# Optimization experiments

Measured on AMD Instinct MI355X. Metric: run time of the kernel, lower is better.

Reference implementation:

```python
import jax, jax.numpy as jnp
import numpy as np

B, S, K = 128, 196, 512   # batch, encoder seq, keys_hidden_size
T_CAP = 16                # caption length (out_seq_len = 15)
V, E, H = 32000, 512, 512 # vocab, embedding, hidden


def setup_inputs() -> dict:
    key = jax.random.key(0)
    ks = jax.random.split(key, 16)
    sc = lambda fan_in: 1.0 / np.sqrt(fan_in)
    return {
        "features": jax.random.normal(ks[0], (B, S, K), jnp.float32),
        "captions": jax.random.randint(ks[1], (B, T_CAP), 0, V),
        "emb": jax.random.normal(ks[2], (V, E), jnp.float32) * 0.02,
        "fc1_w": jax.random.normal(ks[3], (H, E), jnp.float32) * sc(E),
        "fc1_b": jnp.zeros((H,), jnp.float32),
        "att_wq": jax.random.normal(ks[4], (H, H), jnp.float32) * sc(H),
        "att_wk": jax.random.normal(ks[5], (H, K), jnp.float32) * sc(K),
        "att_v": jax.random.normal(ks[6], (H,), jnp.float32) * sc(H),
        "fc0_w": jax.random.normal(ks[7], (H, K), jnp.float32) * sc(K),
        "fc0_b": jnp.zeros((H,), jnp.float32),
        "gru_wih": jax.random.normal(ks[8], (3 * H, 2 * H), jnp.float32) * sc(2 * H),
        "gru_whh": jax.random.normal(ks[9], (3 * H, H), jnp.float32) * sc(H),
        "gru_bih": jnp.zeros((3 * H,), jnp.float32),
        "gru_bhh": jnp.zeros((3 * H,), jnp.float32),
        "fc2_w": jax.random.normal(ks[10], (V, H), jnp.float32) * sc(H),
        "fc2_b": jnp.zeros((V,), jnp.float32),
    }


def reference(features, captions, emb, fc1_w, fc1_b, att_wq, att_wk, att_v,
              fc0_w, fc0_b, gru_wih, gru_whh, gru_bih, gru_bhh, fc2_w, fc2_b):
    # embed captions and project: (B, T_CAP, H)
    x = emb[captions] @ fc1_w.T + fc1_b
    # precompute key projection for Bahdanau attention: (B, S, H)
    keys_proj = features @ att_wk.T

    def step(h, x_t):
        # Bahdanau additive attention
        q = h @ att_wq.T                                   # (B, H)
        scores = jnp.tanh(q[:, None, :] + keys_proj) @ att_v  # (B, S)
        w = jax.nn.softmax(scores, axis=1)
        context = jnp.einsum('bs,bsk->bk', w, features)    # (B, K)
        context = context @ fc0_w.T + fc0_b                # fc_0 -> (B, H)
        rnn_in = jnp.concatenate([x_t, context], axis=-1)  # (B, 2H)
        # GRU cell, torch gate order (r, z, n)
        gi = rnn_in @ gru_wih.T + gru_bih
        gh = h @ gru_whh.T + gru_bhh
        ir, iz, inn = jnp.split(gi, 3, axis=-1)
        hr, hz, hn = jnp.split(gh, 3, axis=-1)
        r = jax.nn.sigmoid(ir + hr)
        z = jax.nn.sigmoid(iz + hz)
        n = jnp.tanh(inn + r * hn)
        h_new = (1.0 - z) * n + z * h
        out = h_new @ fc2_w.T + fc2_b                      # fc_2 -> (B, V)
        return h_new, out

    out_seq_len = captions.shape[1] - 1
    xs = jnp.swapaxes(x[:, :out_seq_len], 0, 1)            # (T, B, H)
    h0 = jnp.zeros((features.shape[0], fc0_b.shape[0]), features.dtype)
    _, outs = jax.lax.scan(step, h0, xs)                   # (T, B, V)
    return jnp.swapaxes(outs, 0, 1)                        # (B, T, V)
```

## Files before the change

### kernel.cpp

```cpp
#include <hip/hip_runtime.h>

typedef _Float16 half_t;
typedef float    floatx4 __attribute__((ext_vector_type(4)));
typedef _Float16 halfx8  __attribute__((ext_vector_type(8)));
typedef _Float16 halfx2  __attribute__((ext_vector_type(2)));

__device__ __forceinline__ float tanh_f(float x) {
  float e = __expf(2.0f * x);
  return 1.0f - 2.0f / (e + 1.0f);
}
__device__ __forceinline__ float sigmoid_f(float x) {
  return 1.0f / (1.0f + __expf(-x));
}

__device__ __forceinline__ void gl16(const void* g, void* s) {
  __builtin_amdgcn_global_load_lds((__attribute__((address_space(1))) unsigned int*)g,
                                   (__attribute__((address_space(3))) unsigned int*)s,
                                   16, 0, 0);
}

__device__ __forceinline__ int xcd_swz(int bid, int nwg) {
  int q = nwg >> 3, r = nwg & 7, x = bid & 7, p = bid >> 3;
  return (x < r ? x * (q + 1) : r * (q + 1) + (x - r) * q) + p;
}

__global__ __launch_bounds__(256) void k_cvt_f16(const float* __restrict__ src,
                                                 half_t* __restrict__ dst, int n) {
  int i = (blockIdx.x * 256 + threadIdx.x) * 4;
  if (i < n) {
    float4 v = *(const float4*)(src + i);
    halfx2 a; a[0] = (half_t)v.x; a[1] = (half_t)v.y;
    halfx2 b; b[0] = (half_t)v.z; b[1] = (half_t)v.w;
    *(halfx2*)(dst + i) = a;
    *(halfx2*)(dst + i + 2) = b;
  }
}

__global__ __launch_bounds__(256) void k_wihsplit(const float* __restrict__ wih,
                                                  half_t* __restrict__ wx,
                                                  half_t* __restrict__ wc) {
  int row = blockIdx.x, j = threadIdx.x * 2;
  float2 a = *(const float2*)(wih + (size_t)row * 1024 + j);
  float2 b = *(const float2*)(wih + (size_t)row * 1024 + 512 + j);
  halfx2 ax; ax[0] = (half_t)a.x; ax[1] = (half_t)a.y;
  halfx2 bx; bx[0] = (half_t)b.x; bx[1] = (half_t)b.y;
  *(halfx2*)(wx + (size_t)row * 512 + j) = ax;
  *(halfx2*)(wc + (size_t)row * 512 + j) = bx;
}

__global__ __launch_bounds__(256) void k_gather(const float* __restrict__ emb,
                                                const int* __restrict__ cap,
                                                half_t* __restrict__ dst) {
  int row = blockIdx.x;
  int b = row / 15, t = row - b * 15;
  int c = cap[b * 16 + t];
  const float* s = emb + (size_t)c * 512;
  int e = threadIdx.x * 2;
  float2 v = *(const float2*)(s + e);
  halfx2 o; o[0] = (half_t)v.x; o[1] = (half_t)v.y;
  *(halfx2*)(dst + (size_t)row * 512 + e) = o;
}

__global__ __launch_bounds__(256) void k_biasc(const float* __restrict__ fc0b,
                                               float* __restrict__ biasc) {
  int i = blockIdx.x * 256 + threadIdx.x;
  biasc[i] = (i < 512) ? 0.f : fc0b[i - 512];
}

__global__ __launch_bounds__(256) void k_zero(float4* p) {
  p[blockIdx.x * 256 + threadIdx.x] = make_float4(0.f, 0.f, 0.f, 0.f);
}

template <bool OUT_F16>
__device__ __forceinline__ void gemm128_body(const half_t* __restrict__ Ap,
                                             const half_t* __restrict__ Bp,
                                             const float* __restrict__ bias,
                                             void* __restrict__ Cp,
                                             const int Kd, const int ldc,
                                             const int m0, const int n0) {
  constexpr int ABYTES = 128 * 32 * 2;
  constexpr int BBYTES = 128 * 32 * 2;
  __shared__ __align__(16) char smem[2 * ABYTES + 2 * BBYTES];

  const int l = threadIdx.x & 63;
  const int w = threadIdx.x >> 6;

  const half_t* gA = Ap + (size_t)(m0 + w * 32 + (l >> 2)) * Kd + (l & 3) * 8;
  const half_t* gB = Bp + (size_t)(n0 + w * 32 + (l >> 2)) * Kd + (l & 3) * 8;

  const int fr = l & 15;
  const int kq = (l >> 4) * 8;
  const int mh = (w & 1) * 64;
  const int nh = (w >> 1) * 64;

  floatx4 acc[4][4];
#pragma unroll
  for (int i = 0; i < 4; ++i)
#pragma unroll
    for (int j = 0; j < 4; ++j) { floatx4 z = {0.f, 0.f, 0.f, 0.f}; acc[i][j] = z; }

  const int NT = Kd >> 5;

  auto stage = [&](int tt) {
    const int k0 = tt * 32;
    char* aD = smem + (tt & 1) * ABYTES;
    char* bD = smem + 2 * ABYTES + (tt & 1) * BBYTES;
    const half_t* g = gA + k0;
    gl16(g, aD + (w * 32) * 64);
    gl16(g + (size_t)16 * Kd, aD + (w * 32 + 16) * 64);
    const half_t* g2 = gB + k0;
    gl16(g2, bD + (w * 32) * 64);
    gl16(g2 + (size_t)16 * Kd, bD + (w * 32 + 16) * 64);
  };

  stage(0);

  for (int t = 0; t < NT; ++t) {
    __syncthreads();
    if (t + 1 < NT) stage(t + 1);
    const char* aB = smem + (t & 1) * ABYTES;
    const char* bB = smem + 2 * ABYTES + (t & 1) * BBYTES;
    halfx8 af[4], bf[4];
#pragma unroll
    for (int i = 0; i < 4; ++i) {
      af[i] = *(const halfx8*)((const half_t*)aB + (size_t)(mh + i * 16 + fr) * 32 + kq);
      bf[i] = *(const halfx8*)((const half_t*)bB + (size_t)(nh + i * 16 + fr) * 32 + kq);
    }
#pragma unroll
    for (int i = 0; i < 4; ++i)
#pragma unroll
      for (int j = 0; j < 4; ++j)
        acc[i][j] = __builtin_amdgcn_mfma_f32_16x16x32_f16(af[i], bf[j], acc[i][j], 0, 0, 0);
  }

#pragma unroll
  for (int j = 0; j < 4; ++j) {
    const int n = n0 + nh + j * 16 + fr;
    const float bv = bias ? bias[n] : 0.0f;
#pragma unroll
    for (int i = 0; i < 4; ++i) {
      const int mb = m0 + mh + i * 16 + (l >> 4) * 4;
#pragma unroll
      for (int r = 0; r < 4; ++r) {
        const float v = acc[i][j][r] + bv;
        const size_t ci = (size_t)(mb + r) * ldc + n;
        if constexpr (OUT_F16) ((half_t*)Cp)[ci] = (half_t)v;
        else                   ((float*)Cp)[ci] = v;
      }
    }
  }
}

template <bool OUT_F16>
__global__ __launch_bounds__(256) void k_gemm_lds(const half_t* __restrict__ Ap,
                                                  const half_t* __restrict__ Bp,
                                                  const float* __restrict__ bias,
                                                  void* __restrict__ Cp,
                                                  int Kd, int ldc) {
  gemm128_body<OUT_F16>(Ap, Bp, bias, Cp, Kd, ldc,
                        blockIdx.y * 128, blockIdx.x * 128);
}

__global__ __launch_bounds__(256) void k_kpfp(const half_t* __restrict__ featf,
                                              const half_t* __restrict__ wkfc0,
                                              const float* __restrict__ biasc,
                                              half_t* __restrict__ kpfp) {
  const int w = (blockIdx.x & 7) * 196 + (blockIdx.x >> 3);
  const int n0 = (w & 7) * 128;
  const int m0 = (w >> 3) * 128;
  gemm128_body<true>(featf, wkfc0, biasc, kpfp, 512, 1024, m0, n0);
}

__global__ __launch_bounds__(256) void k_fc2_final(const half_t* __restrict__ hall,
                                                   const half_t* __restrict__ fc2w,
                                                   const float* __restrict__ fc2b,
                                                   float* __restrict__ outp) {
  const int w = xcd_swz(blockIdx.x, 3750);
  const int m0 = (w % 15) * 128;
  const int n0 = (w / 15) * 128;
  gemm128_body<false>(hall, fc2w, fc2b, outp, 512, 32000, m0, n0);
}

__global__ __launch_bounds__(256) void k_scores(const half_t* __restrict__ kpfp,
                                                const float* __restrict__ ghq,
                                                const float* __restrict__ attv,
                                                float* __restrict__ scores) {
  int w = blockIdx.x * 4 + (threadIdx.x >> 6);
  int l = threadIdx.x & 63;
  int b = w / 196;
  halfx8 kv = *(const halfx8*)(kpfp + (size_t)w * 1024 + l * 8);
  const float* qr = ghq + (size_t)b * 2048 + 1536 + l * 8;
  float4 q0 = *(const float4*)qr;
  float4 q1 = *(const float4*)(qr + 4);
  float4 a0 = *(const float4*)(attv + l * 8);
  float4 a1 = *(const float4*)(attv + l * 8 + 4);
  float acc = a0.x * tanh_f(q0.x + (float)kv[0]);
  acc += a0.y * tanh_f(q0.y + (float)kv[1]);
  acc += a0.z * tanh_f(q0.z + (float)kv[2]);
  acc += a0.w * tanh_f(q0.w + (float)kv[3]);
  acc += a1.x * tanh_f(q1.x + (float)kv[4]);
  acc += a1.y * tanh_f(q1.y + (float)kv[5]);
  acc += a1.z * tanh_f(q1.z + (float)kv[6]);
  acc += a1.w * tanh_f(q1.w + (float)kv[7]);
#pragma unroll
  for (int off = 32; off > 0; off >>= 1) acc += __shfl_xor(acc, off, 64);
  if (l == 0) scores[w] = acc;
}

__global__ __launch_bounds__(256) void k_ctx(const float* __restrict__ scores,
                                             const half_t* __restrict__ kpfp,
                                             half_t* __restrict__ ctxo) {
  const int b = blockIdx.x, kt = blockIdx.y * 128, t = threadIdx.x;
  __shared__ float sw[196], red[256];
  float sc = (t < 196) ? scores[b * 196 + t] : -1e30f;
  red[t] = sc; __syncthreads();
  for (int o = 128; o > 0; o >>= 1) { if (t < o) red[t] = fmaxf(red[t], red[t + o]); __syncthreads(); }
  float mx = red[0]; __syncthreads();
  float e = (t < 196) ? __expf(sc - mx) : 0.f;
  red[t] = e; __syncthreads();
  for (int o = 128; o > 0; o >>= 1) { if (t < o) red[t] += red[t + o]; __syncthreads(); }
  float inv = 1.0f / red[0];
  if (t < 196) sw[t] = e * inv;
  __syncthreads();
  const int kk = t & 127, half = t >> 7, s0 = half * 98;
  const half_t* fp = kpfp + (size_t)(b * 196 + s0) * 1024 + 512 + kt + kk;
  float acc = 0.f;
#pragma unroll 7
  for (int i = 0; i < 98; ++i) acc += sw[s0 + i] * (float)fp[(size_t)i * 1024];
  red[t] = acc; __syncthreads();
  if (t < 128) ctxo[(size_t)b * 512 + kt + t] = (half_t)(red[t] + red[t + 128]);
}

__global__ __launch_bounds__(256) void k_gates(const float* __restrict__ gix,
                                               const float* __restrict__ gic,
                                               const float* __restrict__ ghq,
                                               const float* __restrict__ bih,
                                               const float* __restrict__ bhh,
                                               float* __restrict__ hbuf,
                                               half_t* __restrict__ hh,
                                               half_t* __restrict__ hall, int step) {
  int idx = blockIdx.x * 256 + threadIdx.x;
  int b = idx >> 9, n = idx & 511;
  const float* gx = gix + (size_t)(b * 15 + step) * 1536;
  const float* gc = gic + (size_t)b * 1536;
  const float* gh = ghq + (size_t)b * 2048;
  float ir  = gx[n]        + gc[n]        + bih[n];
  float iz  = gx[n + 512]  + gc[n + 512]  + bih[n + 512];
  float in_ = gx[n + 1024] + gc[n + 1024] + bih[n + 1024];
  float hr  = gh[n]        + bhh[n];
  float hz  = gh[n + 512]  + bhh[n + 512];
  float hn  = gh[n + 1024] + bhh[n + 1024];
  float r = sigmoid_f(ir + hr);
  float z = sigmoid_f(iz + hz);
  float nn = tanh_f(in_ + r * hn);
  float hv = (1.0f - z) * nn + z * hbuf[idx];
  hbuf[idx] = hv;
  half_t h16 = (half_t)hv;
  hh[idx] = h16;
  hall[(size_t)(b * 15 + step) * 512 + n] = h16;
}

extern "C" void kernel_launch(void* const* d_in, const int* in_sizes, int n_in,
                              void* d_out, int out_size, void* d_ws, size_t ws_size,
                              hipStream_t stream) {
  (void)in_sizes; (void)n_in; (void)out_size; (void)ws_size;
  const float* features = (const float*)d_in[0];
  const int*   captions = (const int*)d_in[1];
  const float* emb      = (const float*)d_in[2];
  const float* fc1_w    = (const float*)d_in[3];
  const float* fc1_b    = (const float*)d_in[4];
  const float* att_wq   = (const float*)d_in[5];
  const float* att_wk   = (const float*)d_in[6];
  const float* att_v    = (const float*)d_in[7];
  const float* fc0_w    = (const float*)d_in[8];
  const float* fc0_b    = (const float*)d_in[9];
  const float* gru_wih  = (const float*)d_in[10];
  const float* gru_whh  = (const float*)d_in[11];
  const float* gru_bih  = (const float*)d_in[12];
  const float* gru_bhh  = (const float*)d_in[13];
  const float* fc2_w    = (const float*)d_in[14];
  const float* fc2_b    = (const float*)d_in[15];
  float* out = (float*)d_out;

  char* p = (char*)d_ws;
  half_t* kpfp   = (half_t*)p; p += (size_t)25088 * 1024 * 2;
  half_t* fc2w_h = (half_t*)p; p += (size_t)32000 * 512 * 2;
  float*  gix    = (float*)p;  p += (size_t)1920 * 1536 * 4;
  half_t* wihx_h = (half_t*)p; p += (size_t)1536 * 512 * 2;
  half_t* wihc_h = (half_t*)p; p += (size_t)1536 * 512 * 2;
  half_t* bcat2  = (half_t*)p; p += (size_t)2048 * 512 * 2;
  half_t* wkfc0  = (half_t*)p; p += (size_t)1024 * 512 * 2;
  half_t* fc1w_h = (half_t*)p; p += (size_t)512 * 512 * 2;
  half_t* embg_h = (half_t*)p; p += (size_t)1920 * 512 * 2;
  half_t* xproj_h= (half_t*)p; p += (size_t)1920 * 512 * 2;
  float*  biasc  = (float*)p;  p += (size_t)1024 * 4;
  float*  ghq    = (float*)p;  p += (size_t)128 * 2048 * 4;
  float*  hbuf   = (float*)p;  p += (size_t)128 * 512 * 4;
  float*  scores = (float*)p;  p += (size_t)128 * 196 * 4;
  float*  gic    = (float*)p;  p += (size_t)128 * 1536 * 4;
  half_t* ctxo   = (half_t*)p; p += (size_t)128 * 512 * 2;
  half_t* h_h    = (half_t*)p; p += (size_t)128 * 512 * 2;
  half_t* featf  = (half_t*)p; p += (size_t)25088 * 512 * 2;
  half_t* hall   = (half_t*)p; p += (size_t)1920 * 512 * 2;

  k_cvt_f16<<<dim3(16000), 256, 0, stream>>>(fc2_w, fc2w_h, 32000 * 512);
  k_cvt_f16<<<dim3(12544), 256, 0, stream>>>(features, featf, 25088 * 512);
  k_cvt_f16<<<dim3(256),   256, 0, stream>>>(fc1_w, fc1w_h, 512 * 512);
  k_cvt_f16<<<dim3(256),   256, 0, stream>>>(att_wk, wkfc0, 512 * 512);
  k_cvt_f16<<<dim3(256),   256, 0, stream>>>(fc0_w, wkfc0 + (size_t)512 * 512, 512 * 512);
  k_cvt_f16<<<dim3(768),   256, 0, stream>>>(gru_whh, bcat2, 1536 * 512);
  k_cvt_f16<<<dim3(256),   256, 0, stream>>>(att_wq, bcat2 + (size_t)1536 * 512, 512 * 512);
  k_wihsplit<<<dim3(1536), 256, 0, stream>>>(gru_wih, wihx_h, wihc_h);
  k_gather<<<dim3(1920), 256, 0, stream>>>(emb, captions, embg_h);
  k_biasc<<<dim3(4), 256, 0, stream>>>(fc0_b, biasc);
  k_zero<<<dim3(320), 256, 0, stream>>>((float4*)ghq);
  k_gemm_lds<true><<<dim3(4, 15), 256, 0, stream>>>(embg_h, fc1w_h, fc1_b, xproj_h, 512, 512);
  k_kpfp<<<dim3(1568), 256, 0, stream>>>(featf, wkfc0, biasc, kpfp);
  k_gemm_lds<false><<<dim3(12, 15), 256, 0, stream>>>(xproj_h, wihx_h, nullptr, gix, 512, 1536);

  for (int t = 0; t < 15; ++t) {
    k_scores<<<dim3(6272), 256, 0, stream>>>(kpfp, ghq, att_v, scores);
    k_ctx<<<dim3(128, 4), 256, 0, stream>>>(scores, kpfp, ctxo);
    k_gemm_lds<false><<<dim3(12, 1), 256, 0, stream>>>(ctxo, wihc_h, nullptr, gic, 512, 1536);
    k_gates<<<dim3(256), 256, 0, stream>>>(gix, gic, ghq, gru_bih, gru_bhh, hbuf, h_h, hall, t);
    k_gemm_lds<false><<<dim3(16, 1), 256, 0, stream>>>(h_h, bcat2, nullptr, ghq, 512, 2048);
  }
  k_fc2_final<<<dim3(3750), 256, 0, stream>>>(hall, fc2w_h, fc2_b, out);
}
```

Baseline: 1.206 ms.

## Fuse recurrent decode loop into one persistent kernel with grid barriers

Replaces the 75 per-step launches (scores, context, two small GEMMs, gates) with a single persistent kernel of 128 blocks, one per batch row. The blocks synchronise through an atomic grid barrier placed in the workspace and zeroed by the existing zero kernel. Attention scores, softmax and context for a batch row are now computed inside one block, and the GEMM body takes shared memory as a parameter so it can be reused. This removes launch gaps and intermediate round trips. In exchange the attention phase runs on only 128 CUs, the barriers spin, and correctness relies on all blocks being co-resident.

```diff
diff --git a/kernel.cpp b/kernel.cpp
--- a/kernel.cpp
+++ b/kernel.cpp
@@ -22,6 +22,22 @@
 __device__ __forceinline__ int xcd_swz(int bid, int nwg) {
   int q = nwg >> 3, r = nwg & 7, x = bid & 7, p = bid >> 3;
   return (x < r ? x * (q + 1) : r * (q + 1) + (x - r) * q) + p;
+}
+
+__device__ __forceinline__ void gbar(int* cnt, int* gen, int nb) {
+  __syncthreads();
+  if (threadIdx.x == 0) {
+    int g = __hip_atomic_load(gen, __ATOMIC_RELAXED, __HIP_MEMORY_SCOPE_AGENT);
+    if (__hip_atomic_fetch_add(cnt, 1, __ATOMIC_ACQ_REL, __HIP_MEMORY_SCOPE_AGENT) == nb - 1) {
+      __hip_atomic_store(cnt, 0, __ATOMIC_RELAXED, __HIP_MEMORY_SCOPE_AGENT);
+      __hip_atomic_store(gen, g + 1, __ATOMIC_RELEASE, __HIP_MEMORY_SCOPE_AGENT);
+    } else {
+      while (__hip_atomic_load(gen, __ATOMIC_ACQUIRE, __HIP_MEMORY_SCOPE_AGENT) == g) {
+        __builtin_amdgcn_s_sleep(8);
+      }
+    }
+  }
+  __syncthreads();
 }
 
 __global__ __launch_bounds__(256) void k_cvt_f16(const float* __restrict__ src,
@@ -77,10 +93,10 @@
                                              const float* __restrict__ bias,
                                              void* __restrict__ Cp,
                                              const int Kd, const int ldc,
-                                             const int m0, const int n0) {
+                                             const int m0, const int n0,
+                                             char* smem) {
   constexpr int ABYTES = 128 * 32 * 2;
   constexpr int BBYTES = 128 * 32 * 2;
-  __shared__ __align__(16) char smem[2 * ABYTES + 2 * BBYTES];
 
   const int l = threadIdx.x & 63;
   const int w = threadIdx.x >> 6;
@@ -132,6 +148,7 @@
       for (int j = 0; j < 4; ++j)
         acc[i][j] = __builtin_amdgcn_mfma_f32_16x16x32_f16(af[i], bf[j], acc[i][j], 0, 0, 0);
   }
+  __syncthreads();
 
 #pragma unroll
   for (int j = 0; j < 4; ++j) {
@@ -157,107 +174,142 @@
                                                   const float* __restrict__ bias,
                                                   void* __restrict__ Cp,
                                                   int Kd, int ldc) {
+  __shared__ __align__(16) char smem[32768];
   gemm128_body<OUT_F16>(Ap, Bp, bias, Cp, Kd, ldc,
-                        blockIdx.y * 128, blockIdx.x * 128);
+                        blockIdx.y * 128, blockIdx.x * 128, smem);
 }
 
 __global__ __launch_bounds__(256) void k_kpfp(const half_t* __restrict__ featf,
                                               const half_t* __restrict__ wkfc0,
                                               const float* __restrict__ biasc,
                                               half_t* __restrict__ kpfp) {
+  __shared__ __align__(16) char smem[32768];
   const int w = (blockIdx.x & 7) * 196 + (blockIdx.x >> 3);
   const int n0 = (w & 7) * 128;
   const int m0 = (w >> 3) * 128;
-  gemm128_body<true>(featf, wkfc0, biasc, kpfp, 512, 1024, m0, n0);
+  gemm128_body<true>(featf, wkfc0, biasc, kpfp, 512, 1024, m0, n0, smem);
 }
 
 __global__ __launch_bounds__(256) void k_fc2_final(const half_t* __restrict__ hall,
                                                    const half_t* __restrict__ fc2w,
                                                    const float* __restrict__ fc2b,
                                                    float* __restrict__ outp) {
+  __shared__ __align__(16) char smem[32768];
   const int w = xcd_swz(blockIdx.x, 3750);
   const int m0 = (w % 15) * 128;
   const int n0 = (w / 15) * 128;
-  gemm128_body<false>(hall, fc2w, fc2b, outp, 512, 32000, m0, n0);
-}
-
-__global__ __launch_bounds__(256) void k_scores(const half_t* __restrict__ kpfp,
-                                                const float* __restrict__ ghq,
-                                                const float* __restrict__ attv,
-                                                float* __restrict__ scores) {
-  int w = blockIdx.x * 4 + (threadIdx.x >> 6);
-  int l = threadIdx.x & 63;
-  int b = w / 196;
-  halfx8 kv = *(const halfx8*)(kpfp + (size_t)w * 1024 + l * 8);
-  const float* qr = ghq + (size_t)b * 2048 + 1536 + l * 8;
-  float4 q0 = *(const float4*)qr;
-  float4 q1 = *(const float4*)(qr + 4);
-  float4 a0 = *(const float4*)(attv + l * 8);
-  float4 a1 = *(const float4*)(attv + l * 8 + 4);
-  float acc = a0.x * tanh_f(q0.x + (float)kv[0]);
-  acc += a0.y * tanh_f(q0.y + (float)kv[1]);
-  acc += a0.z * tanh_f(q0.z + (float)kv[2]);
-  acc += a0.w * tanh_f(q0.w + (float)kv[3]);
-  acc += a1.x * tanh_f(q1.x + (float)kv[4]);
-  acc += a1.y * tanh_f(q1.y + (float)kv[5]);
-  acc += a1.z * tanh_f(q1.z + (float)kv[6]);
-  acc += a1.w * tanh_f(q1.w + (float)kv[7]);
-#pragma unroll
-  for (int off = 32; off > 0; off >>= 1) acc += __shfl_xor(acc, off, 64);
-  if (l == 0) scores[w] = acc;
-}
-
-__global__ __launch_bounds__(256) void k_ctx(const float* __restrict__ scores,
-                                             const half_t* __restrict__ kpfp,
-                                             half_t* __restrict__ ctxo) {
-  const int b = blockIdx.x, kt = blockIdx.y * 128, t = threadIdx.x;
-  __shared__ float sw[196], red[256];
-  float sc = (t < 196) ? scores[b * 196 + t] : -1e30f;
-  red[t] = sc; __syncthreads();
-  for (int o = 128; o > 0; o >>= 1) { if (t < o) red[t] = fmaxf(red[t], red[t + o]); __syncthreads(); }
-  float mx = red[0]; __syncthreads();
-  float e = (t < 196) ? __expf(sc - mx) : 0.f;
-  red[t] = e; __syncthreads();
-  for (int o = 128; o > 0; o >>= 1) { if (t < o) red[t] += red[t + o]; __syncthreads(); }
-  float inv = 1.0f / red[0];
-  if (t < 196) sw[t] = e * inv;
-  __syncthreads();
-  const int kk = t & 127, half = t >> 7, s0 = half * 98;
-  const half_t* fp = kpfp + (size_t)(b * 196 + s0) * 1024 + 512 + kt + kk;
-  float acc = 0.f;
-#pragma unroll 7
-  for (int i = 0; i < 98; ++i) acc += sw[s0 + i] * (float)fp[(size_t)i * 1024];
-  red[t] = acc; __syncthreads();
-  if (t < 128) ctxo[(size_t)b * 512 + kt + t] = (half_t)(red[t] + red[t + 128]);
-}
-
-__global__ __launch_bounds__(256) void k_gates(const float* __restrict__ gix,
-                                               const float* __restrict__ gic,
-                                               const float* __restrict__ ghq,
-                                               const float* __restrict__ bih,
-                                               const float* __restrict__ bhh,
-                                               float* __restrict__ hbuf,
-                                               half_t* __restrict__ hh,
-                                               half_t* __restrict__ hall, int step) {
-  int idx = blockIdx.x * 256 + threadIdx.x;
-  int b = idx >> 9, n = idx & 511;
-  const float* gx = gix + (size_t)(b * 15 + step) * 1536;
-  const float* gc = gic + (size_t)b * 1536;
-  const float* gh = ghq + (size_t)b * 2048;
-  float ir  = gx[n]        + gc[n]        + bih[n];
-  float iz  = gx[n + 512]  + gc[n + 512]  + bih[n + 512];
-  float in_ = gx[n + 1024] + gc[n + 1024] + bih[n + 1024];
-  float hr  = gh[n]        + bhh[n];
-  float hz  = gh[n + 512]  + bhh[n + 512];
-  float hn  = gh[n + 1024] + bhh[n + 1024];
-  float r = sigmoid_f(ir + hr);
-  float z = sigmoid_f(iz + hz);
-  float nn = tanh_f(in_ + r * hn);
-  float hv = (1.0f - z) * nn + z * hbuf[idx];
-  hbuf[idx] = hv;
-  half_t h16 = (half_t)hv;
-  hh[idx] = h16;
-  hall[(size_t)(b * 15 + step) * 512 + n] = h16;
+  gemm128_body<false>(hall, fc2w, fc2b, outp, 512, 32000, m0, n0, smem);
+}
+
+__global__ __launch_bounds__(256, 1) void k_decode(const half_t* __restrict__ kpfp,
+                                                   const float* __restrict__ attv,
+                                                   const half_t* __restrict__ wihc,
+                                                   const half_t* __restrict__ bcat2,
+                                                   const float* __restrict__ gix,
+                                                   const float* __restrict__ bih,
+                                                   const float* __restrict__ bhh,
+                                                   float* __restrict__ ghq,
+                                                   float* __restrict__ hbuf,
+                                                   float* __restrict__ gic,
+                                                   half_t* __restrict__ ctxo,
+                                                   half_t* __restrict__ h_h,
+                                                   half_t* __restrict__ hall,
+                                                   int* __restrict__ bar) {
+  __shared__ __align__(16) char smem[32768];
+  const int blk = blockIdx.x, tid = threadIdx.x;
+  const int l = tid & 63, wv = tid >> 6;
+  const int nb = gridDim.x;
+  int* cnt = bar;
+  int* gen = bar + 1;
+
+  for (int t = 0; t < 15; ++t) {
+    {
+      float* sw  = (float*)smem;
+      float* red = (float*)smem + 256;
+      const int b = blk;
+      const float* qr = ghq + (size_t)b * 2048 + 1536 + l * 8;
+      float4 q0 = *(const float4*)qr;
+      float4 q1 = *(const float4*)(qr + 4);
+      float4 a0 = *(const float4*)(attv + l * 8);
+      float4 a1 = *(const float4*)(attv + l * 8 + 4);
+      const half_t* kbase = kpfp + (size_t)b * 196 * 1024 + l * 8;
+      for (int i = 0; i < 49; ++i) {
+        const int s = wv * 49 + i;
+        halfx8 kv = *(const halfx8*)(kbase + (size_t)s * 1024);
+        float acc = a0.x * tanh_f(q0.x + (float)kv[0]);
+        acc += a0.y * tanh_f(q0.y + (float)kv[1]);
+        acc += a0.z * tanh_f(q0.z + (float)kv[2]);
+        acc += a0.w * tanh_f(q0.w + (float)kv[3]);
+        acc += a1.x * tanh_f(q1.x + (float)kv[4]);
+        acc += a1.y * tanh_f(q1.y + (float)kv[5]);
+        acc += a1.z * tanh_f(q1.z + (float)kv[6]);
+        acc += a1.w * tanh_f(q1.w + (float)kv[7]);
+#pragma unroll
+        for (int off = 32; off > 0; off >>= 1) acc += __shfl_xor(acc, off, 64);
+        if (l == 0) sw[s] = acc;
+      }
+      __syncthreads();
+      float sc = (tid < 196) ? sw[tid] : -1e30f;
+      red[tid] = sc; __syncthreads();
+      for (int o = 128; o > 0; o >>= 1) { if (tid < o) red[tid] = fmaxf(red[tid], red[tid + o]); __syncthreads(); }
+      float mx = red[0]; __syncthreads();
+      float e = (tid < 196) ? __expf(sc - mx) : 0.f;
+      red[tid] = e; __syncthreads();
+      for (int o = 128; o > 0; o >>= 1) { if (tid < o) red[tid] += red[tid + o]; __syncthreads(); }
+      float inv = 1.0f / red[0];
+      if (tid < 196) sw[tid] = e * inv;
+      __syncthreads();
+      float c0 = 0.f, c1 = 0.f;
+      const half_t* fp = kpfp + (size_t)b * 196 * 1024 + 512 + tid * 2;
+#pragma unroll 4
+      for (int s = 0; s < 196; ++s) {
+        float wgt = sw[s];
+        halfx2 v = *(const halfx2*)(fp + (size_t)s * 1024);
+        c0 += wgt * (float)v[0];
+        c1 += wgt * (float)v[1];
+      }
+      halfx2 o2; o2[0] = (half_t)c0; o2[1] = (half_t)c1;
+      *(halfx2*)(ctxo + (size_t)b * 512 + tid * 2) = o2;
+    }
+    gbar(cnt, gen, nb);
+
+    if (blk < 12)
+      gemm128_body<false>(ctxo, wihc, nullptr, gic, 512, 1536, 0, blk * 128, smem);
+    gbar(cnt, gen, nb);
+
+    {
+      const int b = blk, n = tid * 2;
+      const float* gx = gix + (size_t)(b * 15 + t) * 1536;
+      const float* gc = gic + (size_t)b * 1536;
+      const float* gh = ghq + (size_t)b * 2048;
+      float2 hv = *(float2*)(hbuf + (size_t)b * 512 + n);
+      float2 res;
+#pragma unroll
+      for (int u = 0; u < 2; ++u) {
+        const int nn = n + u;
+        float ir  = gx[nn]        + gc[nn]        + bih[nn];
+        float iz  = gx[nn + 512]  + gc[nn + 512]  + bih[nn + 512];
+        float in_ = gx[nn + 1024] + gc[nn + 1024] + bih[nn + 1024];
+        float hr  = gh[nn]        + bhh[nn];
+        float hz  = gh[nn + 512]  + bhh[nn + 512];
+        float hn  = gh[nn + 1024] + bhh[nn + 1024];
+        float r = sigmoid_f(ir + hr);
+        float z = sigmoid_f(iz + hz);
+        float g2 = tanh_f(in_ + r * hn);
+        float hnew = (1.0f - z) * g2 + z * (u ? hv.y : hv.x);
+        if (u) res.y = hnew; else res.x = hnew;
+      }
+      *(float2*)(hbuf + (size_t)b * 512 + n) = res;
+      halfx2 h2; h2[0] = (half_t)res.x; h2[1] = (half_t)res.y;
+      *(halfx2*)(h_h + (size_t)b * 512 + n) = h2;
+      *(halfx2*)(hall + (size_t)(b * 15 + t) * 512 + n) = h2;
+    }
+    gbar(cnt, gen, nb);
+
+    if (blk < 16)
+      gemm128_body<false>(h_h, bcat2, nullptr, ghq, 512, 2048, 0, blk * 128, smem);
+    gbar(cnt, gen, nb);
+  }
 }
 
 extern "C" void kernel_launch(void* const* d_in, const int* in_sizes, int n_in,
@@ -296,7 +348,7 @@
   float*  biasc  = (float*)p;  p += (size_t)1024 * 4;
   float*  ghq    = (float*)p;  p += (size_t)128 * 2048 * 4;
   float*  hbuf   = (float*)p;  p += (size_t)128 * 512 * 4;
-  float*  scores = (float*)p;  p += (size_t)128 * 196 * 4;
+  int*    bar    = (int*)p;    p += 16;
   float*  gic    = (float*)p;  p += (size_t)128 * 1536 * 4;
   half_t* ctxo   = (half_t*)p; p += (size_t)128 * 512 * 2;
   half_t* h_h    = (half_t*)p; p += (size_t)128 * 512 * 2;
@@ -313,17 +365,14 @@
   k_wihsplit<<<dim3(1536), 256, 0, stream>>>(gru_wih, wihx_h, wihc_h);
   k_gather<<<dim3(1920), 256, 0, stream>>>(emb, captions, embg_h);
   k_biasc<<<dim3(4), 256, 0, stream>>>(fc0_b, biasc);
-  k_zero<<<dim3(320), 256, 0, stream>>>((float4*)ghq);
+  k_zero<<<dim3(321), 256, 0, stream>>>((float4*)ghq);
   k_gemm_lds<true><<<dim3(4, 15), 256, 0, stream>>>(embg_h, fc1w_h, fc1_b, xproj_h, 512, 512);
   k_kpfp<<<dim3(1568), 256, 0, stream>>>(featf, wkfc0, biasc, kpfp);
   k_gemm_lds<false><<<dim3(12, 15), 256, 0, stream>>>(xproj_h, wihx_h, nullptr, gix, 512, 1536);
 
-  for (int t = 0; t < 15; ++t) {
-    k_scores<<<dim3(6272), 256, 0, stream>>>(kpfp, ghq, att_v, scores);
-    k_ctx<<<dim3(128, 4), 256, 0, stream>>>(scores, kpfp, ctxo);
-    k_gemm_lds<false><<<dim3(12, 1), 256, 0, stream>>>(ctxo, wihc_h, nullptr, gic, 512, 1536);
-    k_gates<<<dim3(256), 256, 0, stream>>>(gix, gic, ghq, gru_bih, gru_bhh, hbuf, h_h, hall, t);
-    k_gemm_lds<false><<<dim3(16, 1), 256, 0, stream>>>(h_h, bcat2, nullptr, ghq, 512, 2048);
-  }
+  k_decode<<<dim3(128), 256, 0, stream>>>(kpfp, att_v, wihc_h, bcat2, gix,
+                                          gru_bih, gru_bhh, ghq, hbuf, gic,
+                                          ctxo, h_h, hall, bar);
+
   k_fc2_final<<<dim3(3750), 256, 0, stream>>>(hall, fc2w_h, fc2_b, out);
 }
```

New measurement: 4.226 ms. +250.3%, slower.

## Fuse attention scores, softmax and context into one per-batch kernel

Applied to the files above, without the earlier changes.

Replaces the separate scores kernel and the softmax+context kernel with a single 1024-thread block per batch row. Scores stay in shared memory instead of round-tripping through global memory, and one launch per timestep is removed. The trade-off is that the scores stage drops from 6272 blocks to only 128 blocks, so fewer CUs are used. The kpfp read is also no longer split across 4 column blocks.

```diff
diff --git a/kernel.cpp b/kernel.cpp
--- a/kernel.cpp
+++ b/kernel.cpp
@@ -181,54 +181,74 @@
   gemm128_body<false>(hall, fc2w, fc2b, outp, 512, 32000, m0, n0);
 }
 
-__global__ __launch_bounds__(256) void k_scores(const half_t* __restrict__ kpfp,
-                                                const float* __restrict__ ghq,
-                                                const float* __restrict__ attv,
-                                                float* __restrict__ scores) {
-  int w = blockIdx.x * 4 + (threadIdx.x >> 6);
-  int l = threadIdx.x & 63;
-  int b = w / 196;
-  halfx8 kv = *(const halfx8*)(kpfp + (size_t)w * 1024 + l * 8);
-  const float* qr = ghq + (size_t)b * 2048 + 1536 + l * 8;
-  float4 q0 = *(const float4*)qr;
-  float4 q1 = *(const float4*)(qr + 4);
-  float4 a0 = *(const float4*)(attv + l * 8);
-  float4 a1 = *(const float4*)(attv + l * 8 + 4);
-  float acc = a0.x * tanh_f(q0.x + (float)kv[0]);
-  acc += a0.y * tanh_f(q0.y + (float)kv[1]);
-  acc += a0.z * tanh_f(q0.z + (float)kv[2]);
-  acc += a0.w * tanh_f(q0.w + (float)kv[3]);
-  acc += a1.x * tanh_f(q1.x + (float)kv[4]);
-  acc += a1.y * tanh_f(q1.y + (float)kv[5]);
-  acc += a1.z * tanh_f(q1.z + (float)kv[6]);
-  acc += a1.w * tanh_f(q1.w + (float)kv[7]);
-#pragma unroll
-  for (int off = 32; off > 0; off >>= 1) acc += __shfl_xor(acc, off, 64);
-  if (l == 0) scores[w] = acc;
-}
-
-__global__ __launch_bounds__(256) void k_ctx(const float* __restrict__ scores,
-                                             const half_t* __restrict__ kpfp,
-                                             half_t* __restrict__ ctxo) {
-  const int b = blockIdx.x, kt = blockIdx.y * 128, t = threadIdx.x;
-  __shared__ float sw[196], red[256];
-  float sc = (t < 196) ? scores[b * 196 + t] : -1e30f;
-  red[t] = sc; __syncthreads();
-  for (int o = 128; o > 0; o >>= 1) { if (t < o) red[t] = fmaxf(red[t], red[t + o]); __syncthreads(); }
+__global__ __launch_bounds__(1024) void k_att(const half_t* __restrict__ kpfp,
+                                              const float* __restrict__ ghq,
+                                              const float* __restrict__ attv,
+                                              half_t* __restrict__ ctxo) {
+  __shared__ float sw[196];
+  __shared__ float red[256];
+  __shared__ float2 rb[1024];
+  const int b = blockIdx.x, tid = threadIdx.x;
+  const int l = tid & 63, wv = tid >> 6;
+
+  {
+    const float* qr = ghq + (size_t)b * 2048 + 1536 + l * 8;
+    float4 q0 = *(const float4*)qr;
+    float4 q1 = *(const float4*)(qr + 4);
+    float4 a0 = *(const float4*)(attv + l * 8);
+    float4 a1 = *(const float4*)(attv + l * 8 + 4);
+    const half_t* kbase = kpfp + (size_t)b * 196 * 1024 + l * 8;
+    for (int s = wv; s < 196; s += 16) {
+      halfx8 kv = *(const halfx8*)(kbase + (size_t)s * 1024);
+      float acc = a0.x * tanh_f(q0.x + (float)kv[0]);
+      acc += a0.y * tanh_f(q0.y + (float)kv[1]);
+      acc += a0.z * tanh_f(q0.z + (float)kv[2]);
+      acc += a0.w * tanh_f(q0.w + (float)kv[3]);
+      acc += a1.x * tanh_f(q1.x + (float)kv[4]);
+      acc += a1.y * tanh_f(q1.y + (float)kv[5]);
+      acc += a1.z * tanh_f(q1.z + (float)kv[6]);
+      acc += a1.w * tanh_f(q1.w + (float)kv[7]);
+#pragma unroll
+      for (int off = 32; off > 0; off >>= 1) acc += __shfl_xor(acc, off, 64);
+      if (l == 0) sw[s] = acc;
+    }
+  }
+  __syncthreads();
+
+  float sc = (tid < 196) ? sw[tid] : -1e30f;
+  if (tid < 256) red[tid] = sc;
+  __syncthreads();
+  for (int o = 128; o > 0; o >>= 1) { if (tid < o) red[tid] = fmaxf(red[tid], red[tid + o]); __syncthreads(); }
   float mx = red[0]; __syncthreads();
-  float e = (t < 196) ? __expf(sc - mx) : 0.f;
-  red[t] = e; __syncthreads();
-  for (int o = 128; o > 0; o >>= 1) { if (t < o) red[t] += red[t + o]; __syncthreads(); }
+  float e = (tid < 196) ? __expf(sc - mx) : 0.f;
+  if (tid < 256) red[tid] = e;
+  __syncthreads();
+  for (int o = 128; o > 0; o >>= 1) { if (tid < o) red[tid] += red[tid + o]; __syncthreads(); }
   float inv = 1.0f / red[0];
-  if (t < 196) sw[t] = e * inv;
-  __syncthreads();
-  const int kk = t & 127, half = t >> 7, s0 = half * 98;
-  const half_t* fp = kpfp + (size_t)(b * 196 + s0) * 1024 + 512 + kt + kk;
-  float acc = 0.f;
+  if (tid < 196) sw[tid] = e * inv;
+  __syncthreads();
+
+  {
+    const int cg = tid & 255, sh = tid >> 8, s0 = sh * 49;
+    const half_t* fp = kpfp + (size_t)(b * 196 + s0) * 1024 + 512 + cg * 2;
+    float c0 = 0.f, c1 = 0.f;
 #pragma unroll 7
-  for (int i = 0; i < 98; ++i) acc += sw[s0 + i] * (float)fp[(size_t)i * 1024];
-  red[t] = acc; __syncthreads();
-  if (t < 128) ctxo[(size_t)b * 512 + kt + t] = (half_t)(red[t] + red[t + 128]);
+    for (int i = 0; i < 49; ++i) {
+      float wgt = sw[s0 + i];
+      halfx2 v = *(const halfx2*)(fp + (size_t)i * 1024);
+      c0 += wgt * (float)v[0];
+      c1 += wgt * (float)v[1];
+    }
+    rb[tid] = make_float2(c0, c1);
+  }
+  __syncthreads();
+  if (tid < 256) {
+    float2 p0 = rb[tid], p1 = rb[tid + 256], p2 = rb[tid + 512], p3 = rb[tid + 768];
+    halfx2 o2;
+    o2[0] = (half_t)(p0.x + p1.x + p2.x + p3.x);
+    o2[1] = (half_t)(p0.y + p1.y + p2.y + p3.y);
+    *(halfx2*)(ctxo + (size_t)b * 512 + tid * 2) = o2;
+  }
 }
 
 __global__ __launch_bounds__(256) void k_gates(const float* __restrict__ gix,
@@ -302,6 +322,7 @@
   half_t* h_h    = (half_t*)p; p += (size_t)128 * 512 * 2;
   half_t* featf  = (half_t*)p; p += (size_t)25088 * 512 * 2;
   half_t* hall   = (half_t*)p; p += (size_t)1920 * 512 * 2;
+  (void)scores;
 
   k_cvt_f16<<<dim3(16000), 256, 0, stream>>>(fc2_w, fc2w_h, 32000 * 512);
   k_cvt_f16<<<dim3(12544), 256, 0, stream>>>(features, featf, 25088 * 512);
@@ -319,8 +340,7 @@
   k_gemm_lds<false><<<dim3(12, 15), 256, 0, stream>>>(xproj_h, wihx_h, nullptr, gix, 512, 1536);
 
   for (int t = 0; t < 15; ++t) {
-    k_scores<<<dim3(6272), 256, 0, stream>>>(kpfp, ghq, att_v, scores);
-    k_ctx<<<dim3(128, 4), 256, 0, stream>>>(scores, kpfp, ctxo);
+    k_att<<<dim3(128), 1024, 0, stream>>>(kpfp, ghq, att_v, ctxo);
     k_gemm_lds<false><<<dim3(12, 1), 256, 0, stream>>>(ctxo, wihc_h, nullptr, gic, 512, 1536);
     k_gates<<<dim3(256), 256, 0, stream>>>(gix, gic, ghq, gru_bih, gru_bhh, hbuf, h_h, hall, t);
     k_gemm_lds<false><<<dim3(16, 1), 256, 0, stream>>>(h_h, bcat2, nullptr, ghq, 512, 2048);
```

After: 1.295 ms. 1.07x slower.
